# Kernel tuning notes

Measured on AMD Instinct MI355X. Metric: run time of the kernel, lower is better.

## Reference

```python
import jax, jax.numpy as jnp
import numpy as np

# ROIAlign config (torchvision semantics, aligned=False)
SPATIAL_SCALE = 0.25
POOLED = 7
SAMPLING_RATIO = 2
MODE = "max"  # from __init__ mode='max'


def setup_inputs() -> dict:
    key = jax.random.key(0)
    kf, kcx, kcy, kw, kh, kb = jax.random.split(key, 6)
    B, C, H, W = 2, 256, 200, 304
    N = 512
    IMG_H, IMG_W = H / SPATIAL_SCALE, W / SPATIAL_SCALE
    feature = jax.random.normal(kf, (B, C, H, W), dtype=jnp.float32)
    cx = jax.random.uniform(kcx, (N,)) * IMG_W
    cy = jax.random.uniform(kcy, (N,)) * IMG_H
    bw = jax.random.uniform(kw, (N,)) * 192.0 + 16.0
    bh = jax.random.uniform(kh, (N,)) * 192.0 + 16.0
    x1 = jnp.clip(cx - bw * 0.5, 0.0, IMG_W - 2.0)
    y1 = jnp.clip(cy - bh * 0.5, 0.0, IMG_H - 2.0)
    x2 = jnp.clip(cx + bw * 0.5, x1 + 1.0, IMG_W - 1.0)
    y2 = jnp.clip(cy + bh * 0.5, y1 + 1.0, IMG_H - 1.0)
    boxes = jnp.stack([x1, y1, x2, y2], axis=1).astype(jnp.float32)
    batch_idx = jax.random.randint(kb, (N,), 0, B, dtype=jnp.int32)
    return {"feature": feature, "boxes": boxes, "batch_idx": batch_idx}


def _sample_coords(start, size):
    # start,size: [N]; returns [N, POOLED*SAMPLING_RATIO] sample coordinates
    bin_sz = size / POOLED                         # [N]
    p = jnp.arange(POOLED, dtype=jnp.float32)      # bin index
    s = (jnp.arange(SAMPLING_RATIO, dtype=jnp.float32) + 0.5) / SAMPLING_RATIO
    # coord = start + (p + s) * bin_sz  -> [N, POOLED, RATIO]
    c = start[:, None, None] + (p[None, :, None] + s[None, None, :]) * bin_sz[:, None, None]
    return c.reshape(c.shape[0], POOLED * SAMPLING_RATIO)


def roi_align(feature, boxes, batch_idx):
    B, C, H, W = feature.shape
    roi = boxes * SPATIAL_SCALE                    # [N,4] in feature coords
    rs_x, rs_y, re_x, re_y = roi[:, 0], roi[:, 1], roi[:, 2], roi[:, 3]
    roi_w = jnp.maximum(re_x - rs_x, 1.0)
    roi_h = jnp.maximum(re_y - rs_y, 1.0)
    ys = _sample_coords(rs_y, roi_h)               # [N, Sy]
    xs = _sample_coords(rs_x, roi_w)               # [N, Sx]
    y = jnp.broadcast_to(ys[:, :, None], (ys.shape[0], ys.shape[1], xs.shape[1]))
    x = jnp.broadcast_to(xs[:, None, :], y.shape)  # [N, Sy, Sx]

    valid = (y > -1.0) & (y < H) & (x > -1.0) & (x < W)
    y = jnp.clip(y, 0.0, H - 1)
    x = jnp.clip(x, 0.0, W - 1)
    y0 = jnp.floor(y).astype(jnp.int32)
    x0 = jnp.floor(x).astype(jnp.int32)
    y1 = jnp.minimum(y0 + 1, H - 1)
    x1 = jnp.minimum(x0 + 1, W - 1)
    ly = y - y0.astype(y.dtype)
    lx = x - x0.astype(x.dtype)
    hy, hx = 1.0 - ly, 1.0 - lx
    b = batch_idx[:, None, None]
    # advanced indexing -> [N, Sy, Sx, C]
    val = (hy * hx)[..., None] * feature[b, :, y0, x0] \
        + (hy * lx)[..., None] * feature[b, :, y0, x1] \
        + (ly * hx)[..., None] * feature[b, :, y1, x0] \
        + (ly * lx)[..., None] * feature[b, :, y1, x1]
    val = jnp.where(valid[..., None], val, 0.0)
    N = boxes.shape[0]
    val = val.reshape(N, POOLED, SAMPLING_RATIO, POOLED, SAMPLING_RATIO, C)
    if MODE == "max":
        out = val.max(axis=(2, 4))                 # [N, PH, PW, C]
    else:
        out = val.mean(axis=(2, 4))
    return jnp.transpose(out, (0, 3, 1, 2))        # [N, C, PH, PW]


def reference(feature, boxes, batch_idx):
    return roi_align(feature, boxes, batch_idx)
```

## Files before the change

kernel.cpp:

```cpp
#include <hip/hip_runtime.h>


#define POOLED 7

constexpr int Cc = 256;
constexpr int Hc = 200;
constexpr int Wc = 304;
constexpr int Nc = 512;
constexpr int PLANE   = Hc * Wc;
constexpr int CELLS   = POOLED * POOLED;
constexpr int PER_BOX = Cc * CELLS;
constexpr int CG      = 4;
constexpr int GRP_B   = 1040;
constexpr int CH_B    = 7 * GRP_B;
constexpr int WSTRIDE = 128;

__device__ __forceinline__ void async_load16(const void* g, void* l) {
    __builtin_amdgcn_global_load_lds(
        (const __attribute__((address_space(1))) unsigned int*)g,
        (__attribute__((address_space(3))) unsigned int*)l, 16, 0, 0);
}

__global__ __launch_bounds__(256) void roi_setup_kernel(
    const float* __restrict__ boxes,
    const int*   __restrict__ batch_idx,
    int*         __restrict__ ws)
{
    int n = blockIdx.x * 4 + (threadIdx.x >> 6);
    int t = threadIdx.x & 63;

    float rsx = boxes[n * 4 + 0] * 0.25f;
    float rsy = boxes[n * 4 + 1] * 0.25f;
    float rex = boxes[n * 4 + 2] * 0.25f;
    float rey = boxes[n * 4 + 3] * 0.25f;
    float bin_w = fmaxf(rex - rsx, 1.0f) / (float)POOLED;
    float bin_h = fmaxf(rey - rsy, 1.0f) / (float)POOLED;

    float xf  = __fadd_rn(rsx, __fmul_rn(0.25f, bin_w));
    float xc0 = fminf(fmaxf(xf, 0.0f), (float)(Wc - 1));
    int xbase = ((int)floorf(xc0)) & ~3;

    int* W = ws + n * WSTRIDE;

    if (t < 14) {
        float px = (float)(t >> 1) + ((float)(t & 1) + 0.5f) * 0.5f;
        float fx = __fadd_rn(rsx, __fmul_rn(px, bin_w));
        bool vx  = (fx > -1.0f) && (fx < (float)Wc);
        float fxc = fminf(fmaxf(fx, 0.0f), (float)(Wc - 1));
        int   x0  = (int)floorf(fxc);
        float lx  = fxc - (float)x0;
        float hx  = 1.0f - lx;
        int4 e;
        e.x = x0 - xbase;
        e.y = min(x0 + 1, Wc - 1) - xbase;
        e.z = __float_as_int(vx ? hx : 0.0f);
        e.w = __float_as_int(vx ? lx : 0.0f);
        *(int4*)(W + 32 + 4 * t) = e;
    } else if (t >= 16 && t < 30) {
        int s = t - 16;
        float py = (float)(s >> 1) + ((float)(s & 1) + 0.5f) * 0.5f;
        float fy = __fadd_rn(rsy, __fmul_rn(py, bin_h));
        bool vy  = (fy > -1.0f) && (fy < (float)Hc);
        float fyc = fminf(fmaxf(fy, 0.0f), (float)(Hc - 1));
        int   y0  = (int)floorf(fyc);
        float ly  = fyc - (float)y0;
        float hy  = 1.0f - ly;
        int2 e;
        e.x = __float_as_int(vy ? hy : 0.0f);
        e.y = __float_as_int(vy ? ly : 0.0f);
        *(int2*)(W + 96 + 2 * s) = e;
    } else if (t >= 32 && t < 60) {
        int slot = t - 32;
        int s    = slot >> 1;
        float py = (float)(s >> 1) + ((float)(s & 1) + 0.5f) * 0.5f;
        float fy = __fadd_rn(rsy, __fmul_rn(py, bin_h));
        float fyc = fminf(fmaxf(fy, 0.0f), (float)(Hc - 1));
        int   y0  = (int)floorf(fyc);
        int   row = (slot & 1) ? min(y0 + 1, Hc - 1) : y0;
        W[slot] = row * (Wc * 4);
    } else if (t == 60) {
        W[28] = xbase;
        W[29] = batch_idx[n];
    }
}

__global__ __launch_bounds__(256) void roi_align_max_kernel(
    const float* __restrict__ feature,
    const int*   __restrict__ ws,
    float*       __restrict__ out)
{
    __shared__ char lds[CG * CH_B];

    int bid = blockIdx.x;
    int xcd = bid & 7;
    int i   = bid >> 3;
    int cg  = (xcd << 3) | (i >> 9);
    int n   = i & 511;

    const int* __restrict__ W = ws + n * WSTRIDE;
    int tid  = threadIdx.x;
    int cl   = tid >> 6;
    int lane = tid & 63;
    int sb   = lane >> 4;
    int l16  = lane & 15;

    int xbase = W[28];
    int b     = W[29];

    int cell = min(lane, 48);
    int ph   = cell / 7;
    int pw   = cell - ph * 7;
    const int4 ex0 = *(const int4*)(W + 32 + 8 * pw);
    const int4 ex1 = *(const int4*)(W + 32 + 8 * pw + 4);
    const int4 eyq = *(const int4*)(W + 96 + 4 * ph);

    const char* gbase = (const char*)(feature
        + ((size_t)b * Cc + (size_t)(cg * CG + cl)) * (size_t)PLANE);
    int colb = min(xbase * 4 + l16 * 16, (Wc - 4) * 4);

    char* lbase = lds + cl * CH_B;
    #pragma unroll
    for (int it = 0; it < 7; ++it) {
        int rowb = W[it * 4 + sb];
        async_load16(gbase + rowb + colb, lbase + it * GRP_B);
    }
    __syncthreads();

    if (lane < CELLS) {
        const float* L = (const float*)(lds + cl * CH_B + ph * GRP_B);
        float wx00 = __int_as_float(ex0.z), wx01 = __int_as_float(ex0.w);
        float wx10 = __int_as_float(ex1.z), wx11 = __int_as_float(ex1.w);
        int c0a = ex0.x, c0b = ex1.x;
        float m = -INFINITY;

        {
            float wy0 = __int_as_float(eyq.x), wy1 = __int_as_float(eyq.y);
            const float* r0 = L;
            const float* r1 = L + 64;
            float a0 = r0[c0a], a1 = r0[c0a + 1];
            float b0 = r1[c0a], b1 = r1[c0a + 1];
            float t0 = fmaf(wx01, a1, wx00 * a0);
            float t1 = fmaf(wx01, b1, wx00 * b0);
            m = fmaxf(m, fmaf(wy1, t1, wy0 * t0));
            float c0_ = r0[c0b], c1_ = r0[c0b + 1];
            float d0 = r1[c0b], d1 = r1[c0b + 1];
            float u0 = fmaf(wx11, c1_, wx10 * c0_);
            float u1 = fmaf(wx11, d1, wx10 * d0);
            m = fmaxf(m, fmaf(wy1, u1, wy0 * u0));
        }
        {
            float wy0 = __int_as_float(eyq.z), wy1 = __int_as_float(eyq.w);
            const float* r0 = L + 128;
            const float* r1 = L + 192;
            float a0 = r0[c0a], a1 = r0[c0a + 1];
            float b0 = r1[c0a], b1 = r1[c0a + 1];
            float t0 = fmaf(wx01, a1, wx00 * a0);
            float t1 = fmaf(wx01, b1, wx00 * b0);
            m = fmaxf(m, fmaf(wy1, t1, wy0 * t0));
            float c0_ = r0[c0b], c1_ = r0[c0b + 1];
            float d0 = r1[c0b], d1 = r1[c0b + 1];
            float u0 = fmaf(wx11, c1_, wx10 * c0_);
            float u1 = fmaf(wx11, d1, wx10 * d0);
            m = fmaxf(m, fmaf(wy1, u1, wy0 * u0));
        }
        out[(size_t)n * PER_BOX + (size_t)(cg * CG + cl) * CELLS + lane] = m;
    }
}

extern "C" void kernel_launch(void* const* d_in, const int* in_sizes, int n_in,
                              void* d_out, int out_size, void* d_ws, size_t ws_size,
                              hipStream_t stream) {
    const float* feature   = (const float*)d_in[0];
    const float* boxes     = (const float*)d_in[1];
    const int*   batch_idx = (const int*)d_in[2];
    float*       out       = (float*)d_out;
    int*         ws        = (int*)d_ws;

    roi_setup_kernel<<<Nc / 4, 256, 0, stream>>>(boxes, batch_idx, ws);

    int grid = (Cc / CG) * Nc;
    roi_align_max_kernel<<<grid, 256, 0, stream>>>(feature, ws, out);
}
```

Baseline: 242.9 us.

## Make ROIAlign blocks persistent over eight channel groups per box

Measured after the change: 258.6 us. +6.5%, slower.

```diff
diff --git a/kernel.cpp b/kernel.cpp
--- a/kernel.cpp
+++ b/kernel.cpp
@@ -11,6 +11,7 @@
 constexpr int CELLS   = POOLED * POOLED;
 constexpr int PER_BOX = Cc * CELLS;
 constexpr int CG      = 4;
+constexpr int ITEMS   = 8;
 constexpr int GRP_B   = 1040;
 constexpr int CH_B    = 7 * GRP_B;
 constexpr int WSTRIDE = 128;
@@ -19,6 +20,10 @@
     __builtin_amdgcn_global_load_lds(
         (const __attribute__((address_space(1))) unsigned int*)g,
         (__attribute__((address_space(3))) unsigned int*)l, 16, 0, 0);
+}
+
+__device__ __forceinline__ void wait_vmcnt0() {
+    __builtin_amdgcn_s_waitcnt(0x0f70);
 }
 
 __global__ __launch_bounds__(256) void roi_setup_kernel(
@@ -91,11 +96,9 @@
 {
     __shared__ char lds[CG * CH_B];
 
-    int bid = blockIdx.x;
-    int xcd = bid & 7;
-    int i   = bid >> 3;
-    int cg  = (xcd << 3) | (i >> 9);
-    int n   = i & 511;
+    int p   = blockIdx.x;
+    int xcd = p & 7;
+    int n   = p >> 3;
 
     const int* __restrict__ W = ws + n * WSTRIDE;
     int tid  = threadIdx.x;
@@ -107,63 +110,76 @@
     int xbase = W[28];
     int b     = W[29];
 
+    int rowb[7];
+    #pragma unroll
+    for (int it = 0; it < 7; ++it)
+        rowb[it] = W[it * 4 + sb];
+
     int cell = min(lane, 48);
     int ph   = cell / 7;
     int pw   = cell - ph * 7;
     const int4 ex0 = *(const int4*)(W + 32 + 8 * pw);
     const int4 ex1 = *(const int4*)(W + 32 + 8 * pw + 4);
     const int4 eyq = *(const int4*)(W + 96 + 4 * ph);
+    float wx00 = __int_as_float(ex0.z), wx01 = __int_as_float(ex0.w);
+    float wx10 = __int_as_float(ex1.z), wx11 = __int_as_float(ex1.w);
+    int c0a = ex0.x, c0b = ex1.x;
 
-    const char* gbase = (const char*)(feature
-        + ((size_t)b * Cc + (size_t)(cg * CG + cl)) * (size_t)PLANE);
     int colb = min(xbase * 4 + l16 * 16, (Wc - 4) * 4);
+    const char* gb = (const char*)feature
+        + ((size_t)b * Cc + (size_t)(xcd * 32 + cl)) * (size_t)PLANE * 4
+        + colb;
+    char* lbase = lds + cl * CH_B;
+    float* op = out + (size_t)n * PER_BOX
+              + (size_t)(xcd * 32 + cl) * CELLS + lane;
 
-    char* lbase = lds + cl * CH_B;
-    #pragma unroll
-    for (int it = 0; it < 7; ++it) {
-        int rowb = W[it * 4 + sb];
-        async_load16(gbase + rowb + colb, lbase + it * GRP_B);
-    }
-    __syncthreads();
+    #pragma unroll 1
+    for (int item = 0; item < ITEMS; ++item) {
+        #pragma unroll
+        for (int it = 0; it < 7; ++it)
+            async_load16(gb + rowb[it], lbase + it * GRP_B);
+        wait_vmcnt0();
+        __syncthreads();
 
-    if (lane < CELLS) {
-        const float* L = (const float*)(lds + cl * CH_B + ph * GRP_B);
-        float wx00 = __int_as_float(ex0.z), wx01 = __int_as_float(ex0.w);
-        float wx10 = __int_as_float(ex1.z), wx11 = __int_as_float(ex1.w);
-        int c0a = ex0.x, c0b = ex1.x;
-        float m = -INFINITY;
+        if (lane < CELLS) {
+            const float* L = (const float*)(lds + cl * CH_B + ph * GRP_B);
+            float m = -INFINITY;
+            {
+                float wy0 = __int_as_float(eyq.x), wy1 = __int_as_float(eyq.y);
+                const float* r0 = L;
+                const float* r1 = L + 64;
+                float a0 = r0[c0a], a1 = r0[c0a + 1];
+                float b0 = r1[c0a], b1 = r1[c0a + 1];
+                float t0 = fmaf(wx01, a1, wx00 * a0);
+                float t1 = fmaf(wx01, b1, wx00 * b0);
+                m = fmaxf(m, fmaf(wy1, t1, wy0 * t0));
+                float c0_ = r0[c0b], c1_ = r0[c0b + 1];
+                float d0 = r1[c0b], d1 = r1[c0b + 1];
+                float u0 = fmaf(wx11, c1_, wx10 * c0_);
+                float u1 = fmaf(wx11, d1, wx10 * d0);
+                m = fmaxf(m, fmaf(wy1, u1, wy0 * u0));
+            }
+            {
+                float wy0 = __int_as_float(eyq.z), wy1 = __int_as_float(eyq.w);
+                const float* r0 = (const float*)(lds + cl * CH_B + ph * GRP_B) + 128;
+                const float* r1 = r0 + 64;
+                float a0 = r0[c0a], a1 = r0[c0a + 1];
+                float b0 = r1[c0a], b1 = r1[c0a + 1];
+                float t0 = fmaf(wx01, a1, wx00 * a0);
+                float t1 = fmaf(wx01, b1, wx00 * b0);
+                m = fmaxf(m, fmaf(wy1, t1, wy0 * t0));
+                float c0_ = r0[c0b], c1_ = r0[c0b + 1];
+                float d0 = r1[c0b], d1 = r1[c0b + 1];
+                float u0 = fmaf(wx11, c1_, wx10 * c0_);
+                float u1 = fmaf(wx11, d1, wx10 * d0);
+                m = fmaxf(m, fmaf(wy1, u1, wy0 * u0));
+            }
+            *op = m;
+        }
+        __syncthreads();
 
-        {
-            float wy0 = __int_as_float(eyq.x), wy1 = __int_as_float(eyq.y);
-            const float* r0 = L;
-            const float* r1 = L + 64;
-            float a0 = r0[c0a], a1 = r0[c0a + 1];
-            float b0 = r1[c0a], b1 = r1[c0a + 1];
-            float t0 = fmaf(wx01, a1, wx00 * a0);
-            float t1 = fmaf(wx01, b1, wx00 * b0);
-            m = fmaxf(m, fmaf(wy1, t1, wy0 * t0));
-            float c0_ = r0[c0b], c1_ = r0[c0b + 1];
-            float d0 = r1[c0b], d1 = r1[c0b + 1];
-            float u0 = fmaf(wx11, c1_, wx10 * c0_);
-            float u1 = fmaf(wx11, d1, wx10 * d0);
-            m = fmaxf(m, fmaf(wy1, u1, wy0 * u0));
-        }
-        {
-            float wy0 = __int_as_float(eyq.z), wy1 = __int_as_float(eyq.w);
-            const float* r0 = L + 128;
-            const float* r1 = L + 192;
-            float a0 = r0[c0a], a1 = r0[c0a + 1];
-            float b0 = r1[c0a], b1 = r1[c0a + 1];
-            float t0 = fmaf(wx01, a1, wx00 * a0);
-            float t1 = fmaf(wx01, b1, wx00 * b0);
-            m = fmaxf(m, fmaf(wy1, t1, wy0 * t0));
-            float c0_ = r0[c0b], c1_ = r0[c0b + 1];
-            float d0 = r1[c0b], d1 = r1[c0b + 1];
-            float u0 = fmaf(wx11, c1_, wx10 * c0_);
-            float u1 = fmaf(wx11, d1, wx10 * d0);
-            m = fmaxf(m, fmaf(wy1, u1, wy0 * u0));
-        }
-        out[(size_t)n * PER_BOX + (size_t)(cg * CG + cl) * CELLS + lane] = m;
+        gb += (size_t)CG * PLANE * 4;
+        op += CG * CELLS;
     }
 }
 
@@ -178,6 +194,6 @@
 
     roi_setup_kernel<<<Nc / 4, 256, 0, stream>>>(boxes, batch_idx, ws);
 
-    int grid = (Cc / CG) * Nc;
+    int grid = 8 * Nc;
     roi_align_max_kernel<<<grid, 256, 0, stream>>>(feature, ws, out);
 }
```
